# Performance work log

Hardware: AMD Instinct MI355X
Metric: run time of the kernel (lower is better)

The kernel has to match this reference:

```python
import jax, jax.numpy as jnp
import numpy as np

FP8 = jnp.float8_e4m3fn

def setup_inputs() -> dict:
    key = jax.random.key(0)
    k_in, k_w = jax.random.split(key)
    M, H = 16384, 4096
    input = jax.random.normal(k_in, (M, H), dtype=jnp.float32)
    # learned fp8 weight, materialized as float32 then quantized in reference
    weight = jax.random.normal(k_w, (H, H), dtype=jnp.float32) * 0.02
    scale_b = jnp.ones((1, H), dtype=jnp.float32)  # per-column dequant scale
    return {"input": input, "weight": weight, "scale_b": scale_b, "world_size": 8}

def reference(input, weight, scale_b, world_size):
    # fp8 quantize input and weight (torch._scaled_mm consumes fp8 operands)
    a = input.astype(FP8).astype(jnp.float32)            # [M, H]
    b = weight.astype(FP8).astype(jnp.float32)           # [H, H]
    scale_a = jnp.ones((input.shape[0], 1), dtype=jnp.float32)  # [M, 1]
    # scaled_mm: (a @ b) * scale_a * scale_b, out_dtype=fp16
    out = (a @ b) * scale_a * scale_b                    # [M, H] fp32 accumulate
    out = out.astype(jnp.float16)
    # reduce_scatter along dim 0: sum corresponding shards across world_size ranks
    M, H = out.shape
    rs = out.reshape(world_size, M // world_size, H).sum(axis=0)  # [M/world, H]
    return rs.astype(jnp.float16)
```

## Files before the change

### kernel.cpp

```cpp
#include <hip/hip_runtime.h>

#define MFULL 16384
#define MOUT  2048
#define H     4096
#define WS    8
#define BK    64
#define BM    128
#define BN    256
#define NT    (H / BK)

typedef _Float16 f16x8 __attribute__((ext_vector_type(8)));
typedef _Float16 f16x4 __attribute__((ext_vector_type(4)));
typedef _Float16 f16x2 __attribute__((ext_vector_type(2)));
typedef float    f32x4 __attribute__((ext_vector_type(4)));
typedef float    f32x2 __attribute__((ext_vector_type(2)));

__device__ __forceinline__ void fp8_rt4(float4& v) {
    int p0 = __builtin_amdgcn_cvt_pk_fp8_f32(v.x, v.y, 0, false);
    int p1 = __builtin_amdgcn_cvt_pk_fp8_f32(v.z, v.w, 0, false);
    f32x2 r0 = __builtin_amdgcn_cvt_pk_f32_fp8(p0, false);
    f32x2 r1 = __builtin_amdgcn_cvt_pk_f32_fp8(p1, false);
    v.x = r0.x; v.y = r0.y; v.z = r1.x; v.w = r1.y;
}

__device__ __forceinline__ void async_copy16(const void* g, void* l) {
    __builtin_amdgcn_global_load_lds(
        (const __attribute__((address_space(1))) void*)g,
        (__attribute__((address_space(3))) void*)l, 16, 0, 0);
}

__global__ void reduce_quant_a(const float* __restrict__ in,
                               _Float16* __restrict__ aq) {
    int idx = blockIdx.x * 256 + threadIdx.x;
    int r = idx >> 10;
    int k = (idx & 1023) * 4;
    const float* p = in + (size_t)r * H + k;
    float4 acc = {0.f, 0.f, 0.f, 0.f};
#pragma unroll
    for (int s = 0; s < WS; ++s) {
        float4 v = *(const float4*)(p + (size_t)s * MOUT * H);
        fp8_rt4(v);
        acc.x += v.x; acc.y += v.y; acc.z += v.z; acc.w += v.w;
    }
    f16x4 h = { (_Float16)acc.x, (_Float16)acc.y, (_Float16)acc.z, (_Float16)acc.w };
    *(f16x4*)(aq + (size_t)r * H + k) = h;
}

__global__ void quant_transpose_b(const float* __restrict__ w,
                                  _Float16* __restrict__ bt) {
    __shared__ _Float16 tile[64][66];
    int t  = threadIdx.x;
    int n0 = blockIdx.x * 64;
    int k0 = blockIdx.y * 64;
#pragma unroll
    for (int i = 0; i < 4; ++i) {
        int lin = i * 256 + t;
        int kl = lin >> 4;
        int nl = (lin & 15) * 4;
        float4 v = *(const float4*)(w + (size_t)(k0 + kl) * H + n0 + nl);
        fp8_rt4(v);
        tile[kl][nl + 0] = (_Float16)v.x;
        tile[kl][nl + 1] = (_Float16)v.y;
        tile[kl][nl + 2] = (_Float16)v.z;
        tile[kl][nl + 3] = (_Float16)v.w;
    }
    __syncthreads();
#pragma unroll
    for (int i = 0; i < 8; ++i) {
        int lin = i * 256 + t;
        int kl = (lin & 31) * 2;
        int nl = lin >> 5;
        f16x2 hv = { tile[kl][nl], tile[kl + 1][nl] };
        *(f16x2*)(bt + (size_t)(n0 + nl) * H + k0 + kl) = hv;
    }
}

__global__ __launch_bounds__(512, 2) void gemm_rs(
    const _Float16* __restrict__ A, const _Float16* __restrict__ Bt,
    const float* __restrict__ scale_b, float* __restrict__ out) {
    __shared__ _Float16 As[3][BM * BK];
    __shared__ _Float16 Bs[3][BN * BK];

    const int tid  = threadIdx.x;
    const int wid  = tid >> 6;
    const int lane = tid & 63;
    const int quad = lane >> 4;
    const int l16  = lane & 15;
    const int bm   = blockIdx.y * BM;
    const int bn   = blockIdx.x * BN;
    const int wm   = (wid >> 2) * 64;
    const int wn   = (wid & 3) * 64;

    f32x4 acc[4][4] = {};

    const _Float16* Ab = A  + (size_t)bm * H;
    const _Float16* Bb = Bt + (size_t)bn * H;

    size_t gaA[2]; int laA[2];
    size_t gaB[4]; int laB[4];
#pragma unroll
    for (int u = 0; u < 2; ++u) {
        int c = u * 512 + tid;
        int row = c >> 3, slot = c & 7;
        int kc = slot ^ ((row >> 1) & 7);
        gaA[u] = (size_t)row * H + kc * 8;
        laA[u] = c * 16;
    }
#pragma unroll
    for (int u = 0; u < 4; ++u) {
        int c = u * 512 + tid;
        int row = c >> 3, slot = c & 7;
        int kc = slot ^ ((row >> 1) & 7);
        gaB[u] = (size_t)row * H + kc * 8;
        laB[u] = c * 16;
    }

    int aOff[4][2], bOff[4][2];
#pragma unroll
    for (int i = 0; i < 4; ++i) {
        int rowA = wm + i * 16 + l16;
        int rowB = wn + i * 16 + l16;
#pragma unroll
        for (int h = 0; h < 2; ++h) {
            int sA = (h * 4 + quad) ^ ((rowA >> 1) & 7);
            int sB = (h * 4 + quad) ^ ((rowB >> 1) & 7);
            aOff[i][h] = rowA * BK + sA * 8;
            bOff[i][h] = rowB * BK + sB * 8;
        }
    }

#define FENCE asm volatile("" ::: "memory")
#define BAR   __builtin_amdgcn_s_barrier()

#define MG(afv, bfv, j)                                                     \
    _Pragma("unroll")                                                       \
    for (int i = 0; i < 4; ++i)                                             \
        acc[i][j] = __builtin_amdgcn_mfma_f32_16x16x32_f16(                 \
            afv[i], bfv, acc[i][j], 0, 0, 0);

#define STAGE_ALL(bufi, koff)                                               \
    {                                                                       \
        char* aL_ = (char*)&As[bufi][0];                                    \
        char* bL_ = (char*)&Bs[bufi][0];                                    \
        _Pragma("unroll")                                                   \
        for (int u = 0; u < 2; ++u)                                         \
            async_copy16(Ab + gaA[u] + (koff), aL_ + laA[u]);               \
        _Pragma("unroll")                                                   \
        for (int u = 0; u < 4; ++u)                                         \
            async_copy16(Bb + gaB[u] + (koff), bL_ + laB[u]);               \
    }

#define COMPUTE_MONO(bufi)                                                  \
    {                                                                       \
        const _Float16* aP_ = &As[bufi][0];                                 \
        const _Float16* bP_ = &Bs[bufi][0];                                 \
        f16x8 af[4][2], bf[4][2];                                           \
        _Pragma("unroll")                                                   \
        for (int i = 0; i < 4; ++i) {                                       \
            _Pragma("unroll")                                               \
            for (int h = 0; h < 2; ++h) {                                   \
                af[i][h] = *(const f16x8*)(aP_ + aOff[i][h]);               \
                bf[i][h] = *(const f16x8*)(bP_ + bOff[i][h]);               \
            }                                                               \
        }                                                                   \
        __builtin_amdgcn_s_setprio(1);                                      \
        _Pragma("unroll")                                                   \
        for (int h = 0; h < 2; ++h)                                         \
            _Pragma("unroll")                                               \
            for (int i = 0; i < 4; ++i)                                     \
                _Pragma("unroll")                                           \
                for (int j = 0; j < 4; ++j)                                 \
                    acc[i][j] = __builtin_amdgcn_mfma_f32_16x16x32_f16(     \
                        af[i][h], bf[j][h], acc[i][j], 0, 0, 0);            \
        __builtin_amdgcn_s_setprio(0);                                      \
    }

    STAGE_ALL(0, 0);
    STAGE_ALL(1, BK);
    asm volatile("s_waitcnt vmcnt(6)" ::: "memory");
    BAR;
    FENCE;

    int cur = 0;
    for (int t = 0; t < NT - 2; ++t) {
        int b2 = cur + 2; if (b2 >= 3) b2 -= 3;
        const _Float16* aP = &As[cur][0];
        const _Float16* bP = &Bs[cur][0];
        char* aL = (char*)&As[b2][0];
        char* bL = (char*)&Bs[b2][0];
        const size_t ko2 = (size_t)(t + 2) * BK;

        f16x8 af0[4], af1[4];

#pragma unroll
        for (int i = 0; i < 4; ++i) af0[i] = *(const f16x8*)(aP + aOff[i][0]);
        f16x8 b00 = *(const f16x8*)(bP + bOff[0][0]);
        f16x8 b10 = *(const f16x8*)(bP + bOff[1][0]);
#pragma unroll
        for (int u = 0; u < 2; ++u) async_copy16(Ab + gaA[u] + ko2, aL + laA[u]);
        FENCE; BAR;
        __builtin_amdgcn_s_setprio(1);
        MG(af0, b00, 0);
        MG(af0, b10, 1);
        __builtin_amdgcn_s_setprio(0);
        FENCE; BAR;

        f16x8 b20 = *(const f16x8*)(bP + bOff[2][0]);
        f16x8 b30 = *(const f16x8*)(bP + bOff[3][0]);
#pragma unroll
        for (int u = 0; u < 2; ++u) async_copy16(Bb + gaB[u] + ko2, bL + laB[u]);
        FENCE; BAR;
        __builtin_amdgcn_s_setprio(1);
        MG(af0, b20, 2);
        MG(af0, b30, 3);
        __builtin_amdgcn_s_setprio(0);
        FENCE; BAR;

#pragma unroll
        for (int i = 0; i < 4; ++i) af1[i] = *(const f16x8*)(aP + aOff[i][1]);
        f16x8 b01 = *(const f16x8*)(bP + bOff[0][1]);
        f16x8 b11 = *(const f16x8*)(bP + bOff[1][1]);
#pragma unroll
        for (int u = 2; u < 4; ++u) async_copy16(Bb + gaB[u] + ko2, bL + laB[u]);
        FENCE; BAR;
        __builtin_amdgcn_s_setprio(1);
        MG(af1, b01, 0);
        MG(af1, b11, 1);
        __builtin_amdgcn_s_setprio(0);
        FENCE; BAR;

        f16x8 b21 = *(const f16x8*)(bP + bOff[2][1]);
        f16x8 b31 = *(const f16x8*)(bP + bOff[3][1]);
        asm volatile("s_waitcnt vmcnt(6)" ::: "memory");
        FENCE; BAR;
        __builtin_amdgcn_s_setprio(1);
        MG(af1, b21, 2);
        MG(af1, b31, 3);
        __builtin_amdgcn_s_setprio(0);
        FENCE; BAR;

        cur = cur + 1; if (cur >= 3) cur = 0;
    }

    COMPUTE_MONO(cur);
    asm volatile("s_waitcnt vmcnt(0)" ::: "memory");
    BAR;
    FENCE;
    cur = cur + 1; if (cur >= 3) cur = 0;
    COMPUTE_MONO(cur);

#undef FENCE
#undef BAR
#undef MG
#undef STAGE_ALL
#undef COMPUTE_MONO

#pragma unroll
    for (int j = 0; j < 4; ++j) {
        int col = bn + wn + j * 16 + l16;
        float sb = scale_b[col];
#pragma unroll
        for (int i = 0; i < 4; ++i) {
#pragma unroll
            for (int r = 0; r < 4; ++r) {
                int row = bm + wm + i * 16 + quad * 4 + r;
                float v = acc[i][j][r] * sb;
                out[(size_t)row * H + col] = (float)(_Float16)v;
            }
        }
    }
}

extern "C" void kernel_launch(void* const* d_in, const int* in_sizes, int n_in,
                              void* d_out, int out_size, void* d_ws, size_t ws_size,
                              hipStream_t stream) {
    const float* input   = (const float*)d_in[0];
    const float* weight  = (const float*)d_in[1];
    const float* scale_b = (const float*)d_in[2];
    float* out = (float*)d_out;

    _Float16* aq = (_Float16*)d_ws;
    _Float16* bt = aq + (size_t)MOUT * H;

    reduce_quant_a<<<(MOUT * H / 4) / 256, 256, 0, stream>>>(input, aq);
    quant_transpose_b<<<dim3(H / 64, H / 64), 256, 0, stream>>>(weight, bt);
    gemm_rs<<<dim3(H / BN, MOUT / BM), 512, 0, stream>>>(aq, bt, scale_b, out);
}
```

Measured before the change: 498.8 us.

## Store transposed weight as fp8 bytes and dequantize B fragments in registers

The quantize-transpose kernel now writes the weight as raw fp8 bytes instead of fp16, which halves the B workspace and the global-to-LDS traffic for B. The GEMM stages B as bytes with a new 16-byte swizzle, issues half as many async copies and matching waitcnt values, and converts each B fragment from fp8 to fp16 in registers before the fp16 MFMA. In exchange it adds per-fragment conversion ALU work inside the main loop, competing with the MFMAs.

```diff
diff --git a/kernel.cpp b/kernel.cpp
--- a/kernel.cpp
+++ b/kernel.cpp
@@ -29,6 +29,20 @@
         (__attribute__((address_space(3))) void*)l, 16, 0, 0);
 }
 
+__device__ __forceinline__ f16x8 bfrag(const unsigned char* p) {
+    const int2 w = *(const int2*)p;
+    f32x2 a = __builtin_amdgcn_cvt_pk_f32_fp8(w.x, false);
+    f32x2 b = __builtin_amdgcn_cvt_pk_f32_fp8(w.x, true);
+    f32x2 c = __builtin_amdgcn_cvt_pk_f32_fp8(w.y, false);
+    f32x2 d = __builtin_amdgcn_cvt_pk_f32_fp8(w.y, true);
+    f16x8 r;
+    r[0] = (_Float16)a.x; r[1] = (_Float16)a.y;
+    r[2] = (_Float16)b.x; r[3] = (_Float16)b.y;
+    r[4] = (_Float16)c.x; r[5] = (_Float16)c.y;
+    r[6] = (_Float16)d.x; r[7] = (_Float16)d.y;
+    return r;
+}
+
 __global__ void reduce_quant_a(const float* __restrict__ in,
                                _Float16* __restrict__ aq) {
     int idx = blockIdx.x * 256 + threadIdx.x;
@@ -47,8 +61,8 @@
 }
 
 __global__ void quant_transpose_b(const float* __restrict__ w,
-                                  _Float16* __restrict__ bt) {
-    __shared__ _Float16 tile[64][66];
+                                  unsigned char* __restrict__ bt) {
+    __shared__ unsigned char tile[64][68];
     int t  = threadIdx.x;
     int n0 = blockIdx.x * 64;
     int k0 = blockIdx.y * 64;
@@ -58,28 +72,29 @@
         int kl = lin >> 4;
         int nl = (lin & 15) * 4;
         float4 v = *(const float4*)(w + (size_t)(k0 + kl) * H + n0 + nl);
-        fp8_rt4(v);
-        tile[kl][nl + 0] = (_Float16)v.x;
-        tile[kl][nl + 1] = (_Float16)v.y;
-        tile[kl][nl + 2] = (_Float16)v.z;
-        tile[kl][nl + 3] = (_Float16)v.w;
+        int p0 = __builtin_amdgcn_cvt_pk_fp8_f32(v.x, v.y, 0, false);
+        int p  = __builtin_amdgcn_cvt_pk_fp8_f32(v.z, v.w, p0, true);
+        tile[nl + 0][kl] = (unsigned char)(p & 0xff);
+        tile[nl + 1][kl] = (unsigned char)((p >> 8) & 0xff);
+        tile[nl + 2][kl] = (unsigned char)((p >> 16) & 0xff);
+        tile[nl + 3][kl] = (unsigned char)((p >> 24) & 0xff);
     }
     __syncthreads();
-#pragma unroll
-    for (int i = 0; i < 8; ++i) {
-        int lin = i * 256 + t;
-        int kl = (lin & 31) * 2;
-        int nl = lin >> 5;
-        f16x2 hv = { tile[kl][nl], tile[kl + 1][nl] };
-        *(f16x2*)(bt + (size_t)(n0 + nl) * H + k0 + kl) = hv;
-    }
+    int n  = t >> 2;
+    int kc = (t & 3) * 16;
+    int4 o;
+    o.x = *(const int*)&tile[n][kc + 0];
+    o.y = *(const int*)&tile[n][kc + 4];
+    o.z = *(const int*)&tile[n][kc + 8];
+    o.w = *(const int*)&tile[n][kc + 12];
+    *(int4*)(bt + (size_t)(n0 + n) * H + k0 + kc) = o;
 }
 
 __global__ __launch_bounds__(512, 2) void gemm_rs(
-    const _Float16* __restrict__ A, const _Float16* __restrict__ Bt,
+    const _Float16* __restrict__ A, const unsigned char* __restrict__ Bt,
     const float* __restrict__ scale_b, float* __restrict__ out) {
-    __shared__ _Float16 As[3][BM * BK];
-    __shared__ _Float16 Bs[3][BN * BK];
+    __shared__ _Float16      As[3][BM * BK];
+    __shared__ unsigned char Bs[3][BN * BK];
 
     const int tid  = threadIdx.x;
     const int wid  = tid >> 6;
@@ -93,11 +108,10 @@
 
     f32x4 acc[4][4] = {};
 
-    const _Float16* Ab = A  + (size_t)bm * H;
-    const _Float16* Bb = Bt + (size_t)bn * H;
+    const _Float16*      Ab = A  + (size_t)bm * H;
+    const unsigned char* Bb = Bt + (size_t)bn * H;
 
     size_t gaA[2]; int laA[2];
-    size_t gaB[4]; int laB[4];
 #pragma unroll
     for (int u = 0; u < 2; ++u) {
         int c = u * 512 + tid;
@@ -106,26 +120,29 @@
         gaA[u] = (size_t)row * H + kc * 8;
         laA[u] = c * 16;
     }
-#pragma unroll
-    for (int u = 0; u < 4; ++u) {
+    size_t gaB[2]; int laB[2];
+#pragma unroll
+    for (int u = 0; u < 2; ++u) {
         int c = u * 512 + tid;
-        int row = c >> 3, slot = c & 7;
-        int kc = slot ^ ((row >> 1) & 7);
-        gaB[u] = (size_t)row * H + kc * 8;
+        int row = c >> 2, slot = c & 3;
+        int g = slot ^ ((row >> 1) & 3);
+        gaB[u] = (size_t)row * H + g * 16;
         laB[u] = c * 16;
     }
 
-    int aOff[4][2], bOff[4][2];
+    int aOff[4][2];
+    int bOff[4][2];
 #pragma unroll
     for (int i = 0; i < 4; ++i) {
         int rowA = wm + i * 16 + l16;
         int rowB = wn + i * 16 + l16;
 #pragma unroll
         for (int h = 0; h < 2; ++h) {
-            int sA = (h * 4 + quad) ^ ((rowA >> 1) & 7);
-            int sB = (h * 4 + quad) ^ ((rowB >> 1) & 7);
+            int q  = h * 4 + quad;
+            int sA = q ^ ((rowA >> 1) & 7);
             aOff[i][h] = rowA * BK + sA * 8;
-            bOff[i][h] = rowB * BK + sB * 8;
+            int s16 = (q >> 1) ^ ((rowB >> 1) & 3);
+            bOff[i][h] = rowB * 64 + s16 * 16 + (q & 1) * 8;
         }
     }
 
@@ -146,21 +163,21 @@
         for (int u = 0; u < 2; ++u)                                         \
             async_copy16(Ab + gaA[u] + (koff), aL_ + laA[u]);               \
         _Pragma("unroll")                                                   \
-        for (int u = 0; u < 4; ++u)                                         \
+        for (int u = 0; u < 2; ++u)                                         \
             async_copy16(Bb + gaB[u] + (koff), bL_ + laB[u]);               \
     }
 
 #define COMPUTE_MONO(bufi)                                                  \
     {                                                                       \
-        const _Float16* aP_ = &As[bufi][0];                                 \
-        const _Float16* bP_ = &Bs[bufi][0];                                 \
+        const _Float16*      aP_ = &As[bufi][0];                            \
+        const unsigned char* bP_ = &Bs[bufi][0];                            \
         f16x8 af[4][2], bf[4][2];                                           \
         _Pragma("unroll")                                                   \
         for (int i = 0; i < 4; ++i) {                                       \
             _Pragma("unroll")                                               \
             for (int h = 0; h < 2; ++h) {                                   \
                 af[i][h] = *(const f16x8*)(aP_ + aOff[i][h]);               \
-                bf[i][h] = *(const f16x8*)(bP_ + bOff[i][h]);               \
+                bf[i][h] = bfrag(bP_ + bOff[i][h]);                         \
             }                                                               \
         }                                                                   \
         __builtin_amdgcn_s_setprio(1);                                      \
@@ -177,15 +194,15 @@
 
     STAGE_ALL(0, 0);
     STAGE_ALL(1, BK);
-    asm volatile("s_waitcnt vmcnt(6)" ::: "memory");
+    asm volatile("s_waitcnt vmcnt(4)" ::: "memory");
     BAR;
     FENCE;
 
     int cur = 0;
     for (int t = 0; t < NT - 2; ++t) {
         int b2 = cur + 2; if (b2 >= 3) b2 -= 3;
-        const _Float16* aP = &As[cur][0];
-        const _Float16* bP = &Bs[cur][0];
+        const _Float16*      aP = &As[cur][0];
+        const unsigned char* bP = &Bs[cur][0];
         char* aL = (char*)&As[b2][0];
         char* bL = (char*)&Bs[b2][0];
         const size_t ko2 = (size_t)(t + 2) * BK;
@@ -194,8 +211,8 @@
 
 #pragma unroll
         for (int i = 0; i < 4; ++i) af0[i] = *(const f16x8*)(aP + aOff[i][0]);
-        f16x8 b00 = *(const f16x8*)(bP + bOff[0][0]);
-        f16x8 b10 = *(const f16x8*)(bP + bOff[1][0]);
+        f16x8 b00 = bfrag(bP + bOff[0][0]);
+        f16x8 b10 = bfrag(bP + bOff[1][0]);
 #pragma unroll
         for (int u = 0; u < 2; ++u) async_copy16(Ab + gaA[u] + ko2, aL + laA[u]);
         FENCE; BAR;
@@ -205,8 +222,8 @@
         __builtin_amdgcn_s_setprio(0);
         FENCE; BAR;
 
-        f16x8 b20 = *(const f16x8*)(bP + bOff[2][0]);
-        f16x8 b30 = *(const f16x8*)(bP + bOff[3][0]);
+        f16x8 b20 = bfrag(bP + bOff[2][0]);
+        f16x8 b30 = bfrag(bP + bOff[3][0]);
 #pragma unroll
         for (int u = 0; u < 2; ++u) async_copy16(Bb + gaB[u] + ko2, bL + laB[u]);
         FENCE; BAR;
@@ -218,10 +235,8 @@
 
 #pragma unroll
         for (int i = 0; i < 4; ++i) af1[i] = *(const f16x8*)(aP + aOff[i][1]);
-        f16x8 b01 = *(const f16x8*)(bP + bOff[0][1]);
-        f16x8 b11 = *(const f16x8*)(bP + bOff[1][1]);
-#pragma unroll
-        for (int u = 2; u < 4; ++u) async_copy16(Bb + gaB[u] + ko2, bL + laB[u]);
+        f16x8 b01 = bfrag(bP + bOff[0][1]);
+        f16x8 b11 = bfrag(bP + bOff[1][1]);
         FENCE; BAR;
         __builtin_amdgcn_s_setprio(1);
         MG(af1, b01, 0);
@@ -229,9 +244,9 @@
         __builtin_amdgcn_s_setprio(0);
         FENCE; BAR;
 
-        f16x8 b21 = *(const f16x8*)(bP + bOff[2][1]);
-        f16x8 b31 = *(const f16x8*)(bP + bOff[3][1]);
-        asm volatile("s_waitcnt vmcnt(6)" ::: "memory");
+        f16x8 b21 = bfrag(bP + bOff[2][1]);
+        f16x8 b31 = bfrag(bP + bOff[3][1]);
+        asm volatile("s_waitcnt vmcnt(4)" ::: "memory");
         FENCE; BAR;
         __builtin_amdgcn_s_setprio(1);
         MG(af1, b21, 2);
@@ -280,7 +295,7 @@
     float* out = (float*)d_out;
 
     _Float16* aq = (_Float16*)d_ws;
-    _Float16* bt = aq + (size_t)MOUT * H;
+    unsigned char* bt = (unsigned char*)d_ws + (size_t)MOUT * H * 2;
 
     reduce_quant_a<<<(MOUT * H / 4) / 256, 256, 0, stream>>>(input, aq);
     quant_transpose_b<<<dim3(H / 64, H / 64), 256, 0, stream>>>(weight, bt);
```

Result: no change. 506.9 us (+1.6%).

## Prefetch next LDS fragments during MFMA groups and drop intermediate barriers

Applied to the files above, without the earlier changes.

Restructures the main K loop so each group of LDS fragment reads is issued one MFMA group earlier, including reading the next stage's first fragments at the end of the current iteration. It also removes the barrier after each MFMA group and keeps only the one before it. The aim is to hide LDS read latency behind matrix core work and cut synchronisation stalls. In exchange it raises register pressure from the fragments kept live across the loop, and it depends on the reordered waitcnt and barrier placement still making the next buffer's data visible before it is read.

```diff
diff --git a/kernel.cpp b/kernel.cpp
--- a/kernel.cpp
+++ b/kernel.cpp
@@ -154,13 +154,13 @@
     {                                                                       \
         const _Float16* aP_ = &As[bufi][0];                                 \
         const _Float16* bP_ = &Bs[bufi][0];                                 \
-        f16x8 af[4][2], bf[4][2];                                           \
+        f16x8 taf[4][2], tbf[4][2];                                         \
         _Pragma("unroll")                                                   \
         for (int i = 0; i < 4; ++i) {                                       \
             _Pragma("unroll")                                               \
             for (int h = 0; h < 2; ++h) {                                   \
-                af[i][h] = *(const f16x8*)(aP_ + aOff[i][h]);               \
-                bf[i][h] = *(const f16x8*)(bP_ + bOff[i][h]);               \
+                taf[i][h] = *(const f16x8*)(aP_ + aOff[i][h]);              \
+                tbf[i][h] = *(const f16x8*)(bP_ + bOff[i][h]);              \
             }                                                               \
         }                                                                   \
         __builtin_amdgcn_s_setprio(1);                                      \
@@ -171,75 +171,90 @@
                 _Pragma("unroll")                                           \
                 for (int j = 0; j < 4; ++j)                                 \
                     acc[i][j] = __builtin_amdgcn_mfma_f32_16x16x32_f16(     \
-                        af[i][h], bf[j][h], acc[i][j], 0, 0, 0);            \
+                        taf[i][h], tbf[j][h], acc[i][j], 0, 0, 0);          \
         __builtin_amdgcn_s_setprio(0);                                      \
     }
+
+    f16x8 af0[4], af1[4];
+    f16x8 b00, b10, b20, b30, b01, b11, b21, b31;
 
     STAGE_ALL(0, 0);
     STAGE_ALL(1, BK);
     asm volatile("s_waitcnt vmcnt(6)" ::: "memory");
     BAR;
     FENCE;
+    {
+        const _Float16* aP = &As[0][0];
+        const _Float16* bP = &Bs[0][0];
+#pragma unroll
+        for (int i = 0; i < 4; ++i) af0[i] = *(const f16x8*)(aP + aOff[i][0]);
+        b00 = *(const f16x8*)(bP + bOff[0][0]);
+        b10 = *(const f16x8*)(bP + bOff[1][0]);
+    }
+    FENCE;
 
     int cur = 0;
     for (int t = 0; t < NT - 2; ++t) {
-        int b2 = cur + 2; if (b2 >= 3) b2 -= 3;
-        const _Float16* aP = &As[cur][0];
-        const _Float16* bP = &Bs[cur][0];
+        int nxt = cur + 1; if (nxt >= 3) nxt -= 3;
+        int b2  = cur + 2; if (b2  >= 3) b2  -= 3;
+        const _Float16* aP  = &As[cur][0];
+        const _Float16* bP  = &Bs[cur][0];
+        const _Float16* aPn = &As[nxt][0];
+        const _Float16* bPn = &Bs[nxt][0];
         char* aL = (char*)&As[b2][0];
         char* bL = (char*)&Bs[b2][0];
         const size_t ko2 = (size_t)(t + 2) * BK;
 
-        f16x8 af0[4], af1[4];
-
-#pragma unroll
-        for (int i = 0; i < 4; ++i) af0[i] = *(const f16x8*)(aP + aOff[i][0]);
-        f16x8 b00 = *(const f16x8*)(bP + bOff[0][0]);
-        f16x8 b10 = *(const f16x8*)(bP + bOff[1][0]);
 #pragma unroll
         for (int u = 0; u < 2; ++u) async_copy16(Ab + gaA[u] + ko2, aL + laA[u]);
+        b20 = *(const f16x8*)(bP + bOff[2][0]);
+        b30 = *(const f16x8*)(bP + bOff[3][0]);
         FENCE; BAR;
         __builtin_amdgcn_s_setprio(1);
         MG(af0, b00, 0);
         MG(af0, b10, 1);
         __builtin_amdgcn_s_setprio(0);
-        FENCE; BAR;
-
-        f16x8 b20 = *(const f16x8*)(bP + bOff[2][0]);
-        f16x8 b30 = *(const f16x8*)(bP + bOff[3][0]);
+        FENCE;
+
 #pragma unroll
         for (int u = 0; u < 2; ++u) async_copy16(Bb + gaB[u] + ko2, bL + laB[u]);
+#pragma unroll
+        for (int i = 0; i < 4; ++i) af1[i] = *(const f16x8*)(aP + aOff[i][1]);
+        b01 = *(const f16x8*)(bP + bOff[0][1]);
+        b11 = *(const f16x8*)(bP + bOff[1][1]);
         FENCE; BAR;
         __builtin_amdgcn_s_setprio(1);
         MG(af0, b20, 2);
         MG(af0, b30, 3);
         __builtin_amdgcn_s_setprio(0);
-        FENCE; BAR;
-
-#pragma unroll
-        for (int i = 0; i < 4; ++i) af1[i] = *(const f16x8*)(aP + aOff[i][1]);
-        f16x8 b01 = *(const f16x8*)(bP + bOff[0][1]);
-        f16x8 b11 = *(const f16x8*)(bP + bOff[1][1]);
+        FENCE;
+
 #pragma unroll
         for (int u = 2; u < 4; ++u) async_copy16(Bb + gaB[u] + ko2, bL + laB[u]);
+        b21 = *(const f16x8*)(bP + bOff[2][1]);
+        b31 = *(const f16x8*)(bP + bOff[3][1]);
+        asm volatile("s_waitcnt vmcnt(6)" ::: "memory");
         FENCE; BAR;
         __builtin_amdgcn_s_setprio(1);
         MG(af1, b01, 0);
         MG(af1, b11, 1);
         __builtin_amdgcn_s_setprio(0);
-        FENCE; BAR;
-
-        f16x8 b21 = *(const f16x8*)(bP + bOff[2][1]);
-        f16x8 b31 = *(const f16x8*)(bP + bOff[3][1]);
-        asm volatile("s_waitcnt vmcnt(6)" ::: "memory");
+        FENCE;
+
+#pragma unroll
+        for (int i = 0; i < 4; ++i) af0[i] = *(const f16x8*)(aPn + aOff[i][0]);
+        b00 = *(const f16x8*)(bPn + bOff[0][0]);
+        b10 = *(const f16x8*)(bPn + bOff[1][0]);
         FENCE; BAR;
         __builtin_amdgcn_s_setprio(1);
         MG(af1, b21, 2);
         MG(af1, b31, 3);
         __builtin_amdgcn_s_setprio(0);
-        FENCE; BAR;
-
-        cur = cur + 1; if (cur >= 3) cur = 0;
+        FENCE;
+        BAR;
+        FENCE;
+
+        cur = nxt;
     }
 
     COMPUTE_MONO(cur);
```

Result: slower. 515.5 us (+3.3%).
